# Optimization experiments

Measured on AMD Instinct MI355X. Metric: run time of the kernel, lower is better.

The kernel has to match this reference:

```python
import jax, jax.numpy as jnp
import numpy as np

N_NODES = 100000
N_EDGES = 625000
D = 128


def setup_inputs() -> dict:
    key = jax.random.key(0)
    ks = jax.random.split(key, 5)
    x = jax.random.normal(ks[0], (N_NODES, D), dtype=jnp.float32)
    edge_index = jax.random.randint(ks[1], (2, N_EDGES), 0, N_NODES, dtype=jnp.int64)
    scale = 1.0 / np.sqrt(D)
    W_neigh = jax.random.normal(ks[2], (D, D), dtype=jnp.float32) * scale
    W_self = jax.random.normal(ks[3], (D, D), dtype=jnp.float32) * scale
    b_self = jax.random.normal(ks[4], (D,), dtype=jnp.float32) * scale
    return {"x": x, "edge_index": edge_index, "W_neigh": W_neigh,
            "W_self": W_self, "b_self": b_self}


def reference(x, edge_index, W_neigh, W_self, b_self):
    src, dst = edge_index[0], edge_index[1]
    n = x.shape[0]
    # mean aggregation over incoming neighbors: segment-sum of x[src] into dst
    neigh = jax.ops.segment_sum(x[src], dst, num_segments=n)  # [N, D]
    counts = jax.ops.segment_sum(jnp.ones((src.shape[0],), dtype=x.dtype), dst,
                                 num_segments=n)  # [N]
    neigh = neigh / jnp.maximum(counts, 1.0)[:, None]
    # lin_self(x) + lin_neigh(neigh); nn.Linear computes x @ W.T + b
    return x @ W_self.T + b_self + neigh @ W_neigh.T
```

## Files before the change

### kernel.cpp

```cpp
#include <hip/hip_runtime.h>
#include <hip/hip_bf16.h>
#include <stdint.h>

#define DFEAT 128
#define CAP 40

typedef __attribute__((ext_vector_type(8))) short short8;
typedef __attribute__((ext_vector_type(4))) float f32x4;

static __device__ __forceinline__ unsigned short f2bf(float f) {
    union { float f; uint32_t u; } v; v.f = f;
    uint32_t u = v.u;
    u += 0x7FFFu + ((u >> 16) & 1u);
    return (unsigned short)(u >> 16);
}

static __device__ __forceinline__ float lo_bf(uint32_t u) {
    union { uint32_t u; float f; } v; v.u = u << 16; return v.f;
}
static __device__ __forceinline__ float hi_bf(uint32_t u) {
    union { uint32_t u; float f; } v; v.u = u & 0xFFFF0000u; return v.f;
}

static __device__ __forceinline__ short8 pack8(const float4& a, const float4& b) {
    short8 r;
    r[0] = (short)f2bf(a.x); r[1] = (short)f2bf(a.y);
    r[2] = (short)f2bf(a.z); r[3] = (short)f2bf(a.w);
    r[4] = (short)f2bf(b.x); r[5] = (short)f2bf(b.y);
    r[6] = (short)f2bf(b.z); r[7] = (short)f2bf(b.w);
    return r;
}

__global__ __launch_bounds__(256) void sage_prep(
    const float* __restrict__ x, unsigned short* __restrict__ xb, int total8,
    const int* __restrict__ ei, int* __restrict__ cur, int* __restrict__ nbr,
    int E) {
    int i = blockIdx.x * 256 + threadIdx.x;
    if (i < E) {
        int s = ei[i];
        int d = ei[E + i];
        int slot = atomicAdd(&cur[d], 1);
        if (slot < CAP) nbr[d * CAP + slot] = s;
    }
    if (i < total8) {
        float4 a = ((const float4*)x)[2 * i];
        float4 b = ((const float4*)x)[2 * i + 1];
        ((short8*)xb)[i] = pack8(a, b);
    }
}

__global__ __launch_bounds__(256) void sage_gather(
    const unsigned short* __restrict__ xb, const int* __restrict__ cur,
    const int* __restrict__ nbr, unsigned short* __restrict__ accb, int N) {
    int t = threadIdx.x;
    int wave = t >> 6;
    int lane = t & 63;
    int grp = lane >> 4;
    int sl = lane & 15;
    int node = blockIdx.x * 16 + wave * 4 + grp;
    if (node >= N) return;

    int degTrue = cur[node];
    int deg = degTrue < CAP ? degTrue : CAP;
    const int* nb = nbr + (size_t)node * CAP;

    float acc[8] = {0.f, 0.f, 0.f, 0.f, 0.f, 0.f, 0.f, 0.f};

    for (int j0 = 0; j0 < deg; j0 += 8) {
        int last = deg - 1;
        int idx[8];
        #pragma unroll
        for (int k = 0; k < 8; ++k) {
            int jj = j0 + k;
            idx[k] = nb[jj < deg ? jj : last];
        }
        uint4 u[8];
        #pragma unroll
        for (int k = 0; k < 8; ++k)
            u[k] = ((const uint4*)(xb + (size_t)idx[k] * DFEAT))[sl];
        #pragma unroll
        for (int k = 0; k < 8; ++k) {
            if (j0 + k < deg) {
                acc[0] += lo_bf(u[k].x); acc[1] += hi_bf(u[k].x);
                acc[2] += lo_bf(u[k].y); acc[3] += hi_bf(u[k].y);
                acc[4] += lo_bf(u[k].z); acc[5] += hi_bf(u[k].z);
                acc[6] += lo_bf(u[k].w); acc[7] += hi_bf(u[k].w);
            }
        }
    }

    float inv = 1.0f / fmaxf((float)degTrue, 1.0f);
    uint4 o;
    o.x = (uint32_t)f2bf(acc[0] * inv) | ((uint32_t)f2bf(acc[1] * inv) << 16);
    o.y = (uint32_t)f2bf(acc[2] * inv) | ((uint32_t)f2bf(acc[3] * inv) << 16);
    o.z = (uint32_t)f2bf(acc[4] * inv) | ((uint32_t)f2bf(acc[5] * inv) << 16);
    o.w = (uint32_t)f2bf(acc[6] * inv) | ((uint32_t)f2bf(acc[7] * inv) << 16);
    ((uint4*)(accb + (size_t)node * DFEAT))[sl] = o;
}

__global__ __launch_bounds__(256) void sage_gemm(
    const unsigned short* __restrict__ xb,
    const unsigned short* __restrict__ accb,
    const float* __restrict__ Ws,
    const float* __restrict__ Wn,
    const float* __restrict__ bias,
    float* __restrict__ out,
    int N, int numTiles) {
    __shared__ unsigned short wlds[128 * 256];

    int t = threadIdx.x;
    #pragma unroll
    for (int it = 0; it < 16; ++it) {
        int id = it * 256 + t;
        int n  = id >> 5;
        int c  = id & 31;
        const float* srcw = (c < 16) ? (Ws + n * 128 + c * 8)
                                     : (Wn + n * 128 + (c - 16) * 8);
        int cs = c ^ (n & 7);
        float4 u0 = *(const float4*)(srcw);
        float4 u1 = *(const float4*)(srcw + 4);
        *(short8*)(wlds + n * 256 + cs * 8) = pack8(u0, u1);
    }
    __syncthreads();

    int lane = t & 63;
    int wave = t >> 6;
    int m = lane & 15;
    int q = lane >> 4;

    for (int tile = blockIdx.x; tile < numTiles; tile += gridDim.x) {
        int arow = tile * 64 + wave * 16 + m;
        bool valid = arow < N;

        short8 afrag[8];
        if (valid) {
            const unsigned short* xr = xb   + (size_t)arow * DFEAT;
            const unsigned short* ar = accb + (size_t)arow * DFEAT;
            #pragma unroll
            for (int tt = 0; tt < 4; ++tt) {
                afrag[tt]     = *(const short8*)(xr + tt * 32 + q * 8);
                afrag[4 + tt] = *(const short8*)(ar + tt * 32 + q * 8);
            }
        } else {
            #pragma unroll
            for (int tt = 0; tt < 8; ++tt) {
                short8 z = {0, 0, 0, 0, 0, 0, 0, 0};
                afrag[tt] = z;
            }
        }

        int orow_base = tile * 64 + wave * 16 + q * 4;
        #pragma unroll
        for (int jt = 0; jt < 8; ++jt) {
            f32x4 c4 = {0.f, 0.f, 0.f, 0.f};
            int n = jt * 16 + m;
            #pragma unroll
            for (int tt = 0; tt < 8; ++tt) {
                int c = tt * 4 + q;
                int cs = c ^ (n & 7);
                short8 bfrag = *(const short8*)(wlds + n * 256 + cs * 8);
                c4 = __builtin_amdgcn_mfma_f32_16x16x32_bf16(afrag[tt], bfrag, c4, 0, 0, 0);
            }
            float bv = bias[n];
            #pragma unroll
            for (int r = 0; r < 4; ++r) {
                int orow = orow_base + r;
                if (orow < N) out[(size_t)orow * DFEAT + n] = c4[r] + bv;
            }
        }
    }
}

extern "C" void kernel_launch(void* const* d_in, const int* in_sizes, int n_in,
                              void* d_out, int out_size, void* d_ws, size_t ws_size,
                              hipStream_t stream) {
    const float* x  = (const float*)d_in[0];
    const int*   ei = (const int*)d_in[1];
    const float* Wn = (const float*)d_in[2];
    const float* Ws = (const float*)d_in[3];
    const float* b  = (const float*)d_in[4];
    float* out = (float*)d_out;

    int N = in_sizes[0] / DFEAT;
    int E = in_sizes[1] / 2;

    int* cur = (int*)d_ws;
    int* nbr = cur + N;
    unsigned short* xbuf = (unsigned short*)(nbr + (size_t)N * CAP);
    unsigned short* accb = xbuf + (size_t)N * DFEAT;

    hipMemsetAsync(cur, 0, (size_t)N * sizeof(int), stream);

    int total8 = N * DFEAT / 8;
    int prepThreads = total8 > E ? total8 : E;
    sage_prep<<<(prepThreads + 255) / 256, 256, 0, stream>>>(
        x, xbuf, total8, ei, cur, nbr, E);
    sage_gather<<<(N + 15) / 16, 256, 0, stream>>>(xbuf, cur, nbr, accb, N);

    int numTiles = (N + 63) / 64;
    sage_gemm<<<512, 256, 0, stream>>>(xbuf, accb, Ws, Wn, b, out, N, numTiles);
}
```

Before: 192.1 us.

## Split prep into fill and convert kernels, enlarge GEMM blocks to 512 threads

The fused prep kernel is split into two kernels. One builds the neighbor lists with two edges per thread. The other converts x to bf16 with a grid-stride loop that issues four loads per thread before storing. The GEMM kernel now runs 512 threads per block over 128-row tiles, so the LDS weight staging is shared by twice as many rows. In exchange there is one extra kernel launch, and the larger GEMM block may lower occupancy.

```diff
diff --git a/kernel.cpp b/kernel.cpp
--- a/kernel.cpp
+++ b/kernel.cpp
@@ -31,21 +31,42 @@
     return r;
 }
 
-__global__ __launch_bounds__(256) void sage_prep(
-    const float* __restrict__ x, unsigned short* __restrict__ xb, int total8,
+__global__ __launch_bounds__(256) void sage_fill(
     const int* __restrict__ ei, int* __restrict__ cur, int* __restrict__ nbr,
-    int E) {
-    int i = blockIdx.x * 256 + threadIdx.x;
-    if (i < E) {
-        int s = ei[i];
-        int d = ei[E + i];
-        int slot = atomicAdd(&cur[d], 1);
-        if (slot < CAP) nbr[d * CAP + slot] = s;
-    }
-    if (i < total8) {
-        float4 a = ((const float4*)x)[2 * i];
-        float4 b = ((const float4*)x)[2 * i + 1];
-        ((short8*)xb)[i] = pack8(a, b);
+    int E, int EH) {
+    int et = blockIdx.x * 256 + threadIdx.x;
+    if (et >= EH) return;
+    int e0 = et;
+    int e1 = et + EH;
+    bool has1 = e1 < E;
+    int s0 = ei[e0];
+    int d0 = ei[E + e0];
+    int s1 = 0, d1 = 0;
+    if (has1) { s1 = ei[e1]; d1 = ei[E + e1]; }
+    int slot0 = atomicAdd(&cur[d0], 1);
+    int slot1 = has1 ? atomicAdd(&cur[d1], 1) : CAP;
+    if (slot0 < CAP) nbr[(size_t)d0 * CAP + slot0] = s0;
+    if (has1 && slot1 < CAP) nbr[(size_t)d1 * CAP + slot1] = s1;
+}
+
+__global__ __launch_bounds__(256) void sage_convert(
+    const float* __restrict__ x, unsigned short* __restrict__ xb, int total8) {
+    int stride = gridDim.x * 256;
+    for (int i = blockIdx.x * 256 + threadIdx.x; i < total8; i += stride * 4) {
+        float4 a[4], b[4];
+        #pragma unroll
+        for (int k = 0; k < 4; ++k) {
+            int j = i + k * stride;
+            if (j < total8) {
+                a[k] = ((const float4*)x)[2 * j];
+                b[k] = ((const float4*)x)[2 * j + 1];
+            }
+        }
+        #pragma unroll
+        for (int k = 0; k < 4; ++k) {
+            int j = i + k * stride;
+            if (j < total8) ((short8*)xb)[j] = pack8(a[k], b[k]);
+        }
     }
 }
 
@@ -98,7 +119,7 @@
     ((uint4*)(accb + (size_t)node * DFEAT))[sl] = o;
 }
 
-__global__ __launch_bounds__(256) void sage_gemm(
+__global__ __launch_bounds__(512) void sage_gemm(
     const unsigned short* __restrict__ xb,
     const unsigned short* __restrict__ accb,
     const float* __restrict__ Ws,
@@ -110,8 +131,8 @@
 
     int t = threadIdx.x;
     #pragma unroll
-    for (int it = 0; it < 16; ++it) {
-        int id = it * 256 + t;
+    for (int it = 0; it < 8; ++it) {
+        int id = it * 512 + t;
         int n  = id >> 5;
         int c  = id & 31;
         const float* srcw = (c < 16) ? (Ws + n * 128 + c * 8)
@@ -129,7 +150,7 @@
     int q = lane >> 4;
 
     for (int tile = blockIdx.x; tile < numTiles; tile += gridDim.x) {
-        int arow = tile * 64 + wave * 16 + m;
+        int arow = tile * 128 + wave * 16 + m;
         bool valid = arow < N;
 
         short8 afrag[8];
@@ -149,7 +170,7 @@
             }
         }
 
-        int orow_base = tile * 64 + wave * 16 + q * 4;
+        int orow_base = tile * 128 + wave * 16 + q * 4;
         #pragma unroll
         for (int jt = 0; jt < 8; ++jt) {
             f32x4 c4 = {0.f, 0.f, 0.f, 0.f};
@@ -191,12 +212,14 @@
 
     hipMemsetAsync(cur, 0, (size_t)N * sizeof(int), stream);
 
+    int EH = (E + 1) / 2;
+    sage_fill<<<(EH + 255) / 256, 256, 0, stream>>>(ei, cur, nbr, E, EH);
+
     int total8 = N * DFEAT / 8;
-    int prepThreads = total8 > E ? total8 : E;
-    sage_prep<<<(prepThreads + 255) / 256, 256, 0, stream>>>(
-        x, xbuf, total8, ei, cur, nbr, E);
+    sage_convert<<<1024, 256, 0, stream>>>(x, xbuf, total8);
+
     sage_gather<<<(N + 15) / 16, 256, 0, stream>>>(xbuf, cur, nbr, accb, N);
 
-    int numTiles = (N + 63) / 64;
-    sage_gemm<<<512, 256, 0, stream>>>(xbuf, accb, Ws, Wn, b, out, N, numTiles);
-}
+    int numTiles = (N + 127) / 128;
+    sage_gemm<<<512, 512, 0, stream>>>(xbuf, accb, Ws, Wn, b, out, N, numTiles);
+}
```

Measured after the change: 226.9 us. +18.1%, slower.
